# Optimization experiments

Measured on AMD Instinct MI355X. Metric: run time of the kernel, lower is better.

## Reference

```python
import jax, jax.numpy as jnp
import numpy as np

N, F_IN, H, C = 100000, 256, 128, 64
E, EP = 1600000, 500000


def setup_inputs() -> dict:
    key = jax.random.key(0)
    ks = jax.random.split(key, 8)
    x = jax.random.normal(ks[0], (N, F_IN), jnp.float32)
    masked_nodes = jax.random.randint(ks[1], (1000,), 0, N)
    pos_edge_index = jax.random.randint(ks[2], (2, EP), 0, N)
    neg_edge_index = jax.random.randint(ks[3], (2, EP), 0, N)
    edge_index = jax.random.randint(ks[4], (2, E), 0, N)
    W1 = jax.random.normal(ks[5], (F_IN, H), jnp.float32) / np.sqrt(F_IN).astype(np.float32)
    b1 = jnp.zeros((H,), jnp.float32)
    W2 = jax.random.normal(ks[6], (H, C), jnp.float32) / np.sqrt(H).astype(np.float32)
    b2 = jnp.zeros((C,), jnp.float32)
    return dict(x=x, masked_nodes=masked_nodes, pos_edge_index=pos_edge_index,
                neg_edge_index=neg_edge_index, edge_index=edge_index,
                W1=W1, b1=b1, W2=W2, b2=b2)


def gcn_conv(x, W, b, src, dst, n):
    # PyG GCNConv: h = x @ W; symmetric norm with self-loops; aggregate; + bias
    h = x @ W  # [N, out]
    deg = jax.ops.segment_sum(jnp.ones(src.shape[0], h.dtype), dst, num_segments=n) + 1.0
    dis = jax.lax.rsqrt(deg)  # D^{-1/2} including self-loop
    msg = h[src] * (dis[src] * dis[dst])[:, None]           # gather + edge-norm
    agg = jax.ops.segment_sum(msg, dst, num_segments=n)      # scatter-add
    agg = agg + h * (dis * dis)[:, None]                      # self-loop term
    return agg + b


def reference(x, masked_nodes, pos_edge_index, neg_edge_index, edge_index, W1, b1, W2, b2):
    n = x.shape[0]
    src, dst = edge_index[0], edge_index[1]
    h = jax.nn.relu(gcn_conv(x, W1, b1, src, dst, n))
    h = gcn_conv(h, W2, b2, src, dst, n)  # [N, C]
    tei = jnp.concatenate([pos_edge_index, neg_edge_index], axis=-1)  # [2, 2*EP]
    x_j = h[tei[0]]  # [2EP, C]
    x_i = h[tei[1]]
    scores = jnp.einsum('ef,ef->e', x_i, x_j)
    return scores, jnp.zeros(tei.shape, jnp.float32)
```

## Files before the change

### kernel.cpp

```cpp
#include <hip/hip_runtime.h>

#define N_NODES 100000
#define F_IN    256
#define H_DIM   128
#define C_DIM   64
#define E_EDGES 1600000
#define EP_EDGES 500000

#define NBUK 391
#define EPB  4096

typedef unsigned short bf16_t;
typedef short  short8  __attribute__((ext_vector_type(8)));
typedef float  float4v __attribute__((ext_vector_type(4)));
typedef _Float16 half8v __attribute__((ext_vector_type(8)));

__device__ inline bf16_t f2bf(float f) {
    unsigned u = __float_as_uint(f);
    u += 0x7fff + ((u >> 16) & 1);
    return (bf16_t)(u >> 16);
}
__device__ inline float bf2f(bf16_t h) {
    return __uint_as_float(((unsigned)h) << 16);
}
__device__ inline void split8(const float* vv, short* h, short* l) {
#pragma unroll
    for (int j = 0; j < 8; ++j) {
        bf16_t hb = f2bf(vv[j]);
        h[j] = (short)hb;
        l[j] = (short)f2bf(vv[j] - bf2f(hb));
    }
}
__device__ inline float4v mfma16(short8 a, short8 b, float4v c) {
    return __builtin_amdgcn_mfma_f32_16x16x32_bf16(a, b, c, 0, 0, 0);
}

__global__ __launch_bounds__(256) void bhist_kernel(const int* __restrict__ dst,
                                                    int* __restrict__ bsize) {
    __shared__ int hist[NBUK];
    const int t = threadIdx.x;
    for (int b = t; b < NBUK; b += 256) hist[b] = 0;
    __syncthreads();
    const int e0 = blockIdx.x * EPB;
#pragma unroll
    for (int i = 0; i < 16; ++i) {
        int e = e0 + i * 256 + t;
        if (e < E_EDGES) atomicAdd(&hist[dst[e] >> 8], 1);
    }
    __syncthreads();
    for (int b = t; b < NBUK; b += 256)
        if (hist[b]) atomicAdd(&bsize[b], hist[b]);
}

__global__ __launch_bounds__(512) void bscan_kernel(const int* __restrict__ bsize,
                                                    int* __restrict__ bbase,
                                                    int* __restrict__ bcursor) {
    __shared__ int sh[512];
    int t = threadIdx.x;
    sh[t] = (t < NBUK) ? bsize[t] : 0;
    __syncthreads();
#pragma unroll
    for (int off = 1; off < 512; off <<= 1) {
        int u = (t >= off) ? sh[t - off] : 0;
        __syncthreads();
        sh[t] += u;
        __syncthreads();
    }
    if (t < NBUK) {
        int ex = (t == 0) ? 0 : sh[t - 1];
        bbase[t] = ex;
        bcursor[t] = ex;
    }
    if (t == 0) bbase[NBUK] = E_EDGES;
}

__global__ __launch_bounds__(256) void bucket_scatter_kernel(const int* __restrict__ src,
                                                             const int* __restrict__ dst,
                                                             int* __restrict__ bcursor,
                                                             int2* __restrict__ pairs) {
    __shared__ int hist[NBUK];
    __shared__ int base[NBUK];
    const int t = threadIdx.x;
    for (int b = t; b < NBUK; b += 256) hist[b] = 0;
    __syncthreads();

    const int e0 = blockIdx.x * EPB;
    int s[16], d[16];
#pragma unroll
    for (int i = 0; i < 16; ++i) {
        int e = e0 + i * 256 + t;
        if (e < E_EDGES) {
            s[i] = src[e];
            d[i] = dst[e];
            atomicAdd(&hist[d[i] >> 8], 1);
        } else {
            d[i] = -1;
        }
    }
    __syncthreads();
    for (int b = t; b < NBUK; b += 256) {
        int c = hist[b];
        base[b] = c ? atomicAdd(&bcursor[b], c) : 0;
        hist[b] = 0;
    }
    __syncthreads();
#pragma unroll
    for (int i = 0; i < 16; ++i) {
        if (d[i] >= 0) {
            int b = d[i] >> 8;
            int r = atomicAdd(&hist[b], 1);
            pairs[base[b] + r] = make_int2(s[i], d[i]);
        }
    }
}

__global__ __launch_bounds__(256) void bucket_sort_kernel(const int2* __restrict__ pairs,
                                                          const int* __restrict__ bbase,
                                                          int* __restrict__ row_ptr,
                                                          float* __restrict__ dis,
                                                          int* __restrict__ csr_src) {
    __shared__ int cnt[256];
    __shared__ int sh[256];
    __shared__ int cur[256];
    const int b = blockIdx.x;
    const int node0 = b << 8;
    const int t = threadIdx.x;
    const int nn = min(256, N_NODES - node0);
    const int beg = bbase[b], end = bbase[b + 1];
    cnt[t] = 0;
    __syncthreads();
    for (int e = beg + t; e < end; e += 256)
        atomicAdd(&cnt[pairs[e].y - node0], 1);
    __syncthreads();
    int c = cnt[t];
    if (t < nn) dis[node0 + t] = rsqrtf((float)c + 1.0f);
    sh[t] = c;
    __syncthreads();
#pragma unroll
    for (int off = 1; off < 256; off <<= 1) {
        int u = (t >= off) ? sh[t - off] : 0;
        __syncthreads();
        sh[t] += u;
        __syncthreads();
    }
    int start = beg + sh[t] - c;
    if (t < nn) row_ptr[node0 + t] = start;
    cur[t] = start;
    if (b == NBUK - 1 && t == 0) row_ptr[N_NODES] = E_EDGES;
    __syncthreads();
    for (int e = beg + t; e < end; e += 256) {
        int2 p = pairs[e];
        int j = atomicAdd(&cur[p.y - node0], 1);
        csr_src[j] = p.x;
    }
}

__global__ __launch_bounds__(256) void wprep_kernel(const float* __restrict__ W1,
                                                    const float* __restrict__ W2,
                                                    short* __restrict__ w1h,
                                                    short* __restrict__ w1l,
                                                    short* __restrict__ w2h,
                                                    short* __restrict__ w2l) {
    int idx = blockIdx.x * 256 + threadIdx.x;
    if (idx < H_DIM * F_IN) {
        int n = idx >> 8, k = idx & 255;
        float w = W1[k * H_DIM + n];
        bf16_t h = f2bf(w);
        w1h[idx] = (short)h;
        w1l[idx] = (short)f2bf(w - bf2f(h));
    }
    int i2 = idx - H_DIM * F_IN;
    if (i2 >= 0 && i2 < C_DIM * H_DIM) {
        int n = i2 >> 7, k = i2 & 127;
        float w = W2[k * C_DIM + n];
        bf16_t h = f2bf(w);
        w2h[i2] = (short)h;
        w2l[i2] = (short)f2bf(w - bf2f(h));
    }
}

#define LSTR 40
__global__ __launch_bounds__(256, 3) void gemm1_mfma(const float* __restrict__ X,
                                                     const short* __restrict__ Wth,
                                                     const short* __restrict__ Wtl,
                                                     const float* __restrict__ dis,
                                                     bf16_t* __restrict__ T,
                                                     int nrows) {
    __shared__ short Bh[128 * LSTR], Bl[128 * LSTR];
    const int t = threadIdx.x;
    const int row0 = blockIdx.x * 128;
    const int w = t >> 6;
    const int lane = t & 63;
    const int m = lane & 15;
    const int q = lane >> 4;
    const int koff = q * 8;

    const int r0 = row0 + w * 32 + m;
    const int r1 = r0 + 16;
    const bool ok0 = r0 < nrows;
    const bool ok1 = r1 < nrows;
    const float* X0 = X + (long long)r0 * F_IN + q * 8;
    const float* X1 = X + (long long)r1 * F_IN + q * 8;

    float4v acc[2][8];
#pragma unroll
    for (int i = 0; i < 2; ++i)
#pragma unroll
        for (int j = 0; j < 8; ++j) acc[i][j] = {0.f, 0.f, 0.f, 0.f};

#pragma unroll 2
    for (int ks = 0; ks < 8; ++ks) {
        const int k0 = ks * 32;
#pragma unroll
        for (int i = 0; i < 2; ++i) {
            int c = t + i * 256;
            int n = c >> 2, kc = c & 3;
            *(short8*)&Bh[n * LSTR + kc * 8] = *(const short8*)&Wth[n * F_IN + k0 + kc * 8];
            *(short8*)&Bl[n * LSTR + kc * 8] = *(const short8*)&Wtl[n * F_IN + k0 + kc * 8];
        }
        float a0[8] = {0.f, 0.f, 0.f, 0.f, 0.f, 0.f, 0.f, 0.f};
        float a1[8] = {0.f, 0.f, 0.f, 0.f, 0.f, 0.f, 0.f, 0.f};
        if (ok0) {
            *(float4*)&a0[0] = *(const float4*)&X0[k0];
            *(float4*)&a0[4] = *(const float4*)&X0[k0 + 4];
        }
        if (ok1) {
            *(float4*)&a1[0] = *(const float4*)&X1[k0];
            *(float4*)&a1[4] = *(const float4*)&X1[k0 + 4];
        }
        short8 ah0, al0, ah1, al1;
        split8(a0, (short*)&ah0, (short*)&al0);
        split8(a1, (short*)&ah1, (short*)&al1);
        __syncthreads();
#pragma unroll
        for (int nc = 0; nc < 8; ++nc) {
            short8 bh = *(const short8*)&Bh[(nc * 16 + m) * LSTR + koff];
            short8 bl = *(const short8*)&Bl[(nc * 16 + m) * LSTR + koff];
            acc[0][nc] = mfma16(ah0, bh, acc[0][nc]);
            acc[0][nc] = mfma16(al0, bh, acc[0][nc]);
            acc[0][nc] = mfma16(ah0, bl, acc[0][nc]);
            acc[1][nc] = mfma16(ah1, bh, acc[1][nc]);
            acc[1][nc] = mfma16(al1, bh, acc[1][nc]);
            acc[1][nc] = mfma16(ah1, bl, acc[1][nc]);
        }
        __syncthreads();
    }
    float ds[2][4];
#pragma unroll
    for (int mt = 0; mt < 2; ++mt)
#pragma unroll
        for (int reg = 0; reg < 4; ++reg) {
            int grow = row0 + w * 32 + mt * 16 + q * 4 + reg;
            ds[mt][reg] = (grow < nrows) ? dis[grow] : 0.f;
        }
#pragma unroll
    for (int mt = 0; mt < 2; ++mt)
#pragma unroll
        for (int nc = 0; nc < 8; ++nc)
#pragma unroll
            for (int reg = 0; reg < 4; ++reg) {
                int grow = row0 + w * 32 + mt * 16 + q * 4 + reg;
                int gcol = nc * 16 + m;
                if (grow < nrows)
                    T[(long long)grow * H_DIM + gcol] = f2bf(acc[mt][nc][reg] * ds[mt][reg]);
            }
}

__global__ __launch_bounds__(256) void gemm2_mfma(const float* __restrict__ A,
                                                  const float* __restrict__ b1,
                                                  const short* __restrict__ Wth,
                                                  const short* __restrict__ Wtl,
                                                  const float* __restrict__ dis,
                                                  bf16_t* __restrict__ T,
                                                  int nrows) {
    __shared__ short Bh[64 * LSTR], Bl[64 * LSTR];
    const int t = threadIdx.x;
    const int row0 = blockIdx.x * 128;
    const int w = t >> 6;
    const int lane = t & 63;
    const int m = lane & 15;
    const int q = lane >> 4;
    const int koff = q * 8;

    const int r0 = row0 + w * 32 + m;
    const int r1 = r0 + 16;
    const bool ok0 = r0 < nrows;
    const bool ok1 = r1 < nrows;
    const float* A0 = A + (long long)r0 * H_DIM + q * 8;
    const float* A1 = A + (long long)r1 * H_DIM + q * 8;
    const float* bp = b1 + q * 8;

    float4v acc[2][4];
#pragma unroll
    for (int i = 0; i < 2; ++i)
#pragma unroll
        for (int j = 0; j < 4; ++j) acc[i][j] = {0.f, 0.f, 0.f, 0.f};

#pragma unroll 2
    for (int ks = 0; ks < 4; ++ks) {
        const int k0 = ks * 32;
        {
            int n = t >> 2, kc = t & 3;
            *(short8*)&Bh[n * LSTR + kc * 8] = *(const short8*)&Wth[n * H_DIM + k0 + kc * 8];
            *(short8*)&Bl[n * LSTR + kc * 8] = *(const short8*)&Wtl[n * H_DIM + k0 + kc * 8];
        }
        float4 bv0 = *(const float4*)&bp[k0];
        float4 bv1 = *(const float4*)&bp[k0 + 4];
        float a0[8] = {0.f, 0.f, 0.f, 0.f, 0.f, 0.f, 0.f, 0.f};
        float a1[8] = {0.f, 0.f, 0.f, 0.f, 0.f, 0.f, 0.f, 0.f};
        if (ok0) {
            float4 v0 = *(const float4*)&A0[k0];
            float4 v1 = *(const float4*)&A0[k0 + 4];
            a0[0] = fmaxf(v0.x + bv0.x, 0.f); a0[1] = fmaxf(v0.y + bv0.y, 0.f);
            a0[2] = fmaxf(v0.z + bv0.z, 0.f); a0[3] = fmaxf(v0.w + bv0.w, 0.f);
            a0[4] = fmaxf(v1.x + bv1.x, 0.f); a0[5] = fmaxf(v1.y + bv1.y, 0.f);
            a0[6] = fmaxf(v1.z + bv1.z, 0.f); a0[7] = fmaxf(v1.w + bv1.w, 0.f);
        }
        if (ok1) {
            float4 v0 = *(const float4*)&A1[k0];
            float4 v1 = *(const float4*)&A1[k0 + 4];
            a1[0] = fmaxf(v0.x + bv0.x, 0.f); a1[1] = fmaxf(v0.y + bv0.y, 0.f);
            a1[2] = fmaxf(v0.z + bv0.z, 0.f); a1[3] = fmaxf(v0.w + bv0.w, 0.f);
            a1[4] = fmaxf(v1.x + bv1.x, 0.f); a1[5] = fmaxf(v1.y + bv1.y, 0.f);
            a1[6] = fmaxf(v1.z + bv1.z, 0.f); a1[7] = fmaxf(v1.w + bv1.w, 0.f);
        }
        short8 ah0, al0, ah1, al1;
        split8(a0, (short*)&ah0, (short*)&al0);
        split8(a1, (short*)&ah1, (short*)&al1);
        __syncthreads();
#pragma unroll
        for (int nc = 0; nc < 4; ++nc) {
            short8 bh = *(const short8*)&Bh[(nc * 16 + m) * LSTR + koff];
            short8 bl = *(const short8*)&Bl[(nc * 16 + m) * LSTR + koff];
            acc[0][nc] = mfma16(ah0, bh, acc[0][nc]);
            acc[0][nc] = mfma16(al0, bh, acc[0][nc]);
            acc[0][nc] = mfma16(ah0, bl, acc[0][nc]);
            acc[1][nc] = mfma16(ah1, bh, acc[1][nc]);
            acc[1][nc] = mfma16(al1, bh, acc[1][nc]);
            acc[1][nc] = mfma16(ah1, bl, acc[1][nc]);
        }
        __syncthreads();
    }
    float ds[2][4];
#pragma unroll
    for (int mt = 0; mt < 2; ++mt)
#pragma unroll
        for (int reg = 0; reg < 4; ++reg) {
            int grow = row0 + w * 32 + mt * 16 + q * 4 + reg;
            ds[mt][reg] = (grow < nrows) ? dis[grow] : 0.f;
        }
#pragma unroll
    for (int mt = 0; mt < 2; ++mt)
#pragma unroll
        for (int nc = 0; nc < 4; ++nc)
#pragma unroll
            for (int reg = 0; reg < 4; ++reg) {
                int grow = row0 + w * 32 + mt * 16 + q * 4 + reg;
                int gcol = nc * 16 + m;
                if (grow < nrows)
                    T[(long long)grow * C_DIM + gcol] = f2bf(acc[mt][nc][reg] * ds[mt][reg]);
            }
}

__device__ inline void add8_bf16(float* acc, uint4 u) {
#pragma unroll
    for (int p = 0; p < 4; ++p) {
        unsigned w = (&u.x)[p];
        acc[2 * p]     += __uint_as_float(w << 16);
        acc[2 * p + 1] += __uint_as_float(w & 0xffff0000u);
    }
}

template <int CS, bool HAS_BIAS, bool F16OUT>
__global__ __launch_bounds__(256) void agg_kernel(const bf16_t* __restrict__ t,
                                                  const float* __restrict__ dis,
                                                  const int* __restrict__ row_ptr,
                                                  const int* __restrict__ csr_src,
                                                  const float* __restrict__ bias,
                                                  float* __restrict__ aggf,
                                                  _Float16* __restrict__ aggh) {
    unsigned idx = blockIdx.x * 256u + threadIdx.x;
    if (idx >= (unsigned)(N_NODES << CS)) return;
    int node = idx >> CS;
    int q = idx & ((1 << CS) - 1);
    const uint4* tv = (const uint4*)t;
    int beg = row_ptr[node], end = row_ptr[node + 1];

    float acc[8];
    {
        uint4 u = tv[idx];
#pragma unroll
        for (int p = 0; p < 4; ++p) {
            unsigned w = (&u.x)[p];
            acc[2 * p]     = __uint_as_float(w << 16);
            acc[2 * p + 1] = __uint_as_float(w & 0xffff0000u);
        }
    }

    int j = beg;
    for (; j + 3 < end; j += 4) {
        int s0 = csr_src[j + 0], s1 = csr_src[j + 1];
        int s2 = csr_src[j + 2], s3 = csr_src[j + 3];
        uint4 u0 = tv[((unsigned)s0 << CS) + q];
        uint4 u1 = tv[((unsigned)s1 << CS) + q];
        uint4 u2 = tv[((unsigned)s2 << CS) + q];
        uint4 u3 = tv[((unsigned)s3 << CS) + q];
        add8_bf16(acc, u0);
        add8_bf16(acc, u1);
        add8_bf16(acc, u2);
        add8_bf16(acc, u3);
    }
    for (; j < end; ++j) {
        int s = csr_src[j];
        add8_bf16(acc, tv[((unsigned)s << CS) + q]);
    }

    float dd = dis[node];
#pragma unroll
    for (int p = 0; p < 8; ++p) acc[p] *= dd;

    if (HAS_BIAS) {
        float4 bv0 = ((const float4*)bias)[q * 2];
        float4 bv1 = ((const float4*)bias)[q * 2 + 1];
        acc[0] += bv0.x; acc[1] += bv0.y; acc[2] += bv0.z; acc[3] += bv0.w;
        acc[4] += bv1.x; acc[5] += bv1.y; acc[6] += bv1.z; acc[7] += bv1.w;
    }
    if (F16OUT) {
        half8v hv;
#pragma unroll
        for (int p = 0; p < 8; ++p) hv[p] = (_Float16)acc[p];
        ((half8v*)aggh)[idx] = hv;
    } else {
        float4 o0 = make_float4(acc[0], acc[1], acc[2], acc[3]);
        float4 o1 = make_float4(acc[4], acc[5], acc[6], acc[7]);
        ((float4*)aggf)[idx * 2]     = o0;
        ((float4*)aggf)[idx * 2 + 1] = o1;
    }
}

__global__ __launch_bounds__(256) void score_kernel(const _Float16* __restrict__ h2,
                                                    const int* __restrict__ pos,
                                                    const int* __restrict__ neg,
                                                    float* __restrict__ out) {
    int tid = blockIdx.x * 256 + threadIdx.x;
    int e = tid >> 3;
    int q = tid & 7;
    if (e >= 2 * EP_EDGES) return;
    int i, j;
    if (e < EP_EDGES) {
        j = pos[e];
        i = pos[EP_EDGES + e];
    } else {
        j = neg[e - EP_EDGES];
        i = neg[e];
    }
    half8v a = ((const half8v*)h2)[i * 8 + q];
    half8v b = ((const half8v*)h2)[j * 8 + q];
    float v = 0.f;
#pragma unroll
    for (int k = 0; k < 8; ++k) v = fmaf((float)a[k], (float)b[k], v);
    v += __shfl_down(v, 4, 8);
    v += __shfl_down(v, 2, 8);
    v += __shfl_down(v, 1, 8);
    if (q == 0) out[e] = v;
}

extern "C" void kernel_launch(void* const* d_in, const int* in_sizes, int n_in,
                              void* d_out, int out_size, void* d_ws, size_t ws_size,
                              hipStream_t stream) {
    const float* x  = (const float*)d_in[0];
    const int* pos  = (const int*)d_in[2];
    const int* neg  = (const int*)d_in[3];
    const int* ei   = (const int*)d_in[4];
    const float* W1 = (const float*)d_in[5];
    const float* b1 = (const float*)d_in[6];
    const float* W2 = (const float*)d_in[7];
    const float* b2 = (const float*)d_in[8];
    float* out = (float*)d_out;

    char* ws = (char*)d_ws;
    float*  dis     = (float*) (ws + 0);
    int*    row_ptr = (int*)   (ws + 400000);
    int*    bsize   = (int*)   (ws + 800128);
    int*    bbase   = (int*)   (ws + 801792);
    int*    bcursor = (int*)   (ws + 803456);
    int*    csr_src = (int*)   (ws + 805120);
    int2*   pairs   = (int2*)  (ws + 7205120);
    _Float16* h2f16 = (_Float16*)(ws + 7205120);
    bf16_t* t       = (bf16_t*)(ws + 20005120);
    float*  agg     = (float*) (ws + 45605120);
    short*  w1th    = (short*) (ws + 96805120);
    short*  w1tl    = (short*) (ws + 96870656);
    short*  w2th    = (short*) (ws + 96936192);
    short*  w2tl    = (short*) (ws + 96952576);

    const int* esrc = ei;
    const int* edst = ei + E_EDGES;

    hipMemsetAsync(bsize, 0, NBUK * sizeof(int), stream);
    bhist_kernel<<<(E_EDGES + EPB - 1) / EPB, 256, 0, stream>>>(edst, bsize);
    bscan_kernel<<<1, 512, 0, stream>>>(bsize, bbase, bcursor);
    bucket_scatter_kernel<<<(E_EDGES + EPB - 1) / EPB, 256, 0, stream>>>(
        esrc, edst, bcursor, pairs);
    bucket_sort_kernel<<<NBUK, 256, 0, stream>>>(pairs, bbase, row_ptr, dis, csr_src);
    wprep_kernel<<<(H_DIM * F_IN + C_DIM * H_DIM + 255) / 256, 256, 0, stream>>>(
        W1, W2, w1th, w1tl, w2th, w2tl);

    gemm1_mfma<<<(N_NODES + 127) / 128, 256, 0, stream>>>(x, w1th, w1tl, dis, t, N_NODES);
    agg_kernel<4, false, false><<<(N_NODES * 16 + 255) / 256, 256, 0, stream>>>(
        t, dis, row_ptr, csr_src, nullptr, agg, nullptr);

    gemm2_mfma<<<(N_NODES + 127) / 128, 256, 0, stream>>>(agg, b1, w2th, w2tl, dis, t, N_NODES);
    agg_kernel<3, true, true><<<(N_NODES * 8 + 255) / 256, 256, 0, stream>>>(
        t, dis, row_ptr, csr_src, b2, nullptr, h2f16);

    score_kernel<<<(2 * EP_EDGES * 8) / 256, 256, 0, stream>>>(h2f16, pos, neg, out);

    hipMemsetAsync(out + 2 * EP_EDGES, 0, (size_t)4 * EP_EDGES * sizeof(float), stream);
}
```

Baseline: 403.3 us.

## Double-buffer GEMM weight tiles via direct global-to-LDS loads with swizzled layout

Both MFMA GEMM kernels now double-buffer the weight tiles in LDS and prefetch the next K-slice of weights and activations while the current slice is computed, dropping one barrier per iteration. Weight staging uses the global_load_lds builtin so data goes straight into shared memory without passing through registers. To avoid LDS bank conflicts without padding, the weight prep kernel writes an XOR-swizzled column order that the readers undo. This costs more LDS and registers per block and gives gemm2 a 3-block occupancy hint, and the overall gain is limited because the GEMMs are only part of a pipeline that also includes graph aggregation.

```diff
diff --git a/kernel.cpp b/kernel.cpp
--- a/kernel.cpp
+++ b/kernel.cpp
@@ -34,6 +34,12 @@
 __device__ inline float4v mfma16(short8 a, short8 b, float4v c) {
     return __builtin_amdgcn_mfma_f32_16x16x32_bf16(a, b, c, 0, 0, 0);
 }
+__device__ inline void gload_lds16(const void* gptr, void* lptr) {
+    __builtin_amdgcn_global_load_lds(
+        (const __attribute__((address_space(1))) unsigned int*)gptr,
+        (__attribute__((address_space(3))) unsigned int*)lptr, 16, 0, 0);
+}
+#define XSWZ(nn) (((nn) >> 1) & 3)
 
 __global__ __launch_bounds__(256) void bhist_kernel(const int* __restrict__ dst,
                                                     int* __restrict__ bsize) {
@@ -164,36 +170,58 @@
     int idx = blockIdx.x * 256 + threadIdx.x;
     if (idx < H_DIM * F_IN) {
         int n = idx >> 8, k = idx & 255;
+        int kc = (k >> 3) & 3;
+        int dk = (k & ~0x18) | (((kc ^ XSWZ(n)) & 3) << 3);
         float w = W1[k * H_DIM + n];
         bf16_t h = f2bf(w);
-        w1h[idx] = (short)h;
-        w1l[idx] = (short)f2bf(w - bf2f(h));
+        w1h[n * F_IN + dk] = (short)h;
+        w1l[n * F_IN + dk] = (short)f2bf(w - bf2f(h));
     }
     int i2 = idx - H_DIM * F_IN;
     if (i2 >= 0 && i2 < C_DIM * H_DIM) {
         int n = i2 >> 7, k = i2 & 127;
+        int kc = (k >> 3) & 3;
+        int dk = (k & ~0x18) | (((kc ^ XSWZ(n)) & 3) << 3);
         float w = W2[k * C_DIM + n];
         bf16_t h = f2bf(w);
-        w2h[i2] = (short)h;
-        w2l[i2] = (short)f2bf(w - bf2f(h));
-    }
-}
-
-#define LSTR 40
+        w2h[n * H_DIM + dk] = (short)h;
+        w2l[n * H_DIM + dk] = (short)f2bf(w - bf2f(h));
+    }
+}
+
+#define G1_STAGE(BUF, KSN)                                                     \
+    for (int i_ = 0; i_ < 2; ++i_) {                                           \
+        int e_ = t + i_ * 256;                                                 \
+        gload_lds16(&Wth[(e_ >> 2) * F_IN + (KSN) * 32 + (e_ & 3) * 8],        \
+                    &Bh[(BUF) * 4096 + e_ * 8]);                               \
+        gload_lds16(&Wtl[(e_ >> 2) * F_IN + (KSN) * 32 + (e_ & 3) * 8],        \
+                    &Bl[(BUF) * 4096 + e_ * 8]);                               \
+    }
+
+#define G1_LOADA(BANK, KSN)                                                    \
+    if (ok0) {                                                                 \
+        *(float4*)&aP[BANK][0][0] = *(const float4*)&X0[(KSN) * 32];           \
+        *(float4*)&aP[BANK][0][4] = *(const float4*)&X0[(KSN) * 32 + 4];       \
+    }                                                                          \
+    if (ok1) {                                                                 \
+        *(float4*)&aP[BANK][1][0] = *(const float4*)&X1[(KSN) * 32];           \
+        *(float4*)&aP[BANK][1][4] = *(const float4*)&X1[(KSN) * 32 + 4];       \
+    }
+
 __global__ __launch_bounds__(256, 3) void gemm1_mfma(const float* __restrict__ X,
                                                      const short* __restrict__ Wth,
                                                      const short* __restrict__ Wtl,
                                                      const float* __restrict__ dis,
                                                      bf16_t* __restrict__ T,
                                                      int nrows) {
-    __shared__ short Bh[128 * LSTR], Bl[128 * LSTR];
+    __shared__ short Bh[2 * 4096], Bl[2 * 4096];
     const int t = threadIdx.x;
     const int row0 = blockIdx.x * 128;
     const int w = t >> 6;
     const int lane = t & 63;
     const int m = lane & 15;
     const int q = lane >> 4;
-    const int koff = q * 8;
+    const int qs = ((q ^ XSWZ(m)) & 3) << 3;
 
     const int r0 = row0 + w * 32 + m;
     const int r1 = r0 + 16;
@@ -208,34 +236,27 @@
 #pragma unroll
         for (int j = 0; j < 8; ++j) acc[i][j] = {0.f, 0.f, 0.f, 0.f};
 
-#pragma unroll 2
+    float aP[2][2][8] = {};
+
+    G1_STAGE(0, 0)
+    G1_LOADA(0, 0)
+    __syncthreads();
+
+#pragma unroll
     for (int ks = 0; ks < 8; ++ks) {
-        const int k0 = ks * 32;
-#pragma unroll
-        for (int i = 0; i < 2; ++i) {
-            int c = t + i * 256;
-            int n = c >> 2, kc = c & 3;
-            *(short8*)&Bh[n * LSTR + kc * 8] = *(const short8*)&Wth[n * F_IN + k0 + kc * 8];
-            *(short8*)&Bl[n * LSTR + kc * 8] = *(const short8*)&Wtl[n * F_IN + k0 + kc * 8];
-        }
-        float a0[8] = {0.f, 0.f, 0.f, 0.f, 0.f, 0.f, 0.f, 0.f};
-        float a1[8] = {0.f, 0.f, 0.f, 0.f, 0.f, 0.f, 0.f, 0.f};
-        if (ok0) {
-            *(float4*)&a0[0] = *(const float4*)&X0[k0];
-            *(float4*)&a0[4] = *(const float4*)&X0[k0 + 4];
-        }
-        if (ok1) {
-            *(float4*)&a1[0] = *(const float4*)&X1[k0];
-            *(float4*)&a1[4] = *(const float4*)&X1[k0 + 4];
+        const int p = ks & 1;
+        if (ks < 7) {
+            G1_STAGE(p ^ 1, ks + 1)
+            G1_LOADA(p ^ 1, ks + 1)
         }
         short8 ah0, al0, ah1, al1;
-        split8(a0, (short*)&ah0, (short*)&al0);
-        split8(a1, (short*)&ah1, (short*)&al1);
-        __syncthreads();
+        split8(aP[p][0], (short*)&ah0, (short*)&al0);
+        split8(aP[p][1], (short*)&ah1, (short*)&al1);
 #pragma unroll
         for (int nc = 0; nc < 8; ++nc) {
-            short8 bh = *(const short8*)&Bh[(nc * 16 + m) * LSTR + koff];
-            short8 bl = *(const short8*)&Bl[(nc * 16 + m) * LSTR + koff];
+            const int bo = p * 4096 + (nc * 16 + m) * 32 + qs;
+            short8 bh = *(const short8*)&Bh[bo];
+            short8 bl = *(const short8*)&Bl[bo];
             acc[0][nc] = mfma16(ah0, bh, acc[0][nc]);
             acc[0][nc] = mfma16(al0, bh, acc[0][nc]);
             acc[0][nc] = mfma16(ah0, bl, acc[0][nc]);
@@ -245,13 +266,13 @@
         }
         __syncthreads();
     }
-    float ds[2][4];
+    float ds_[2][4];
 #pragma unroll
     for (int mt = 0; mt < 2; ++mt)
 #pragma unroll
         for (int reg = 0; reg < 4; ++reg) {
             int grow = row0 + w * 32 + mt * 16 + q * 4 + reg;
-            ds[mt][reg] = (grow < nrows) ? dis[grow] : 0.f;
+            ds_[mt][reg] = (grow < nrows) ? dis[grow] : 0.f;
         }
 #pragma unroll
     for (int mt = 0; mt < 2; ++mt)
@@ -262,25 +283,41 @@
                 int grow = row0 + w * 32 + mt * 16 + q * 4 + reg;
                 int gcol = nc * 16 + m;
                 if (grow < nrows)
-                    T[(long long)grow * H_DIM + gcol] = f2bf(acc[mt][nc][reg] * ds[mt][reg]);
+                    T[(long long)grow * H_DIM + gcol] = f2bf(acc[mt][nc][reg] * ds_[mt][reg]);
             }
 }
 
-__global__ __launch_bounds__(256) void gemm2_mfma(const float* __restrict__ A,
-                                                  const float* __restrict__ b1,
-                                                  const short* __restrict__ Wth,
-                                                  const short* __restrict__ Wtl,
-                                                  const float* __restrict__ dis,
-                                                  bf16_t* __restrict__ T,
-                                                  int nrows) {
-    __shared__ short Bh[64 * LSTR], Bl[64 * LSTR];
+#define G2_STAGE(BUF, KSN)                                                     \
+    gload_lds16(&Wth[(t >> 2) * H_DIM + (KSN) * 32 + (t & 3) * 8],             \
+                &Bh[(BUF) * 2048 + t * 8]);                                    \
+    gload_lds16(&Wtl[(t >> 2) * H_DIM + (KSN) * 32 + (t & 3) * 8],             \
+                &Bl[(BUF) * 2048 + t * 8]);
+
+#define G2_LOADA(BANK, KSN)                                                    \
+    if (ok0) {                                                                 \
+        *(float4*)&aP[BANK][0][0] = *(const float4*)&A0[(KSN) * 32];           \
+        *(float4*)&aP[BANK][0][4] = *(const float4*)&A0[(KSN) * 32 + 4];       \
+    }                                                                          \
+    if (ok1) {                                                                 \
+        *(float4*)&aP[BANK][1][0] = *(const float4*)&A1[(KSN) * 32];           \
+        *(float4*)&aP[BANK][1][4] = *(const float4*)&A1[(KSN) * 32 + 4];       \
+    }
+
+__global__ __launch_bounds__(256, 3) void gemm2_mfma(const float* __restrict__ A,
+                                                     const float* __restrict__ b1,
+                                                     const short* __restrict__ Wth,
+                                                     const short* __restrict__ Wtl,
+                                                     const float* __restrict__ dis,
+                                                     bf16_t* __restrict__ T,
+                                                     int nrows) {
+    __shared__ short Bh[2 * 2048], Bl[2 * 2048];
     const int t = threadIdx.x;
     const int row0 = blockIdx.x * 128;
     const int w = t >> 6;
     const int lane = t & 63;
     const int m = lane & 15;
     const int q = lane >> 4;
-    const int koff = q * 8;
+    const int qs = ((q ^ XSWZ(m)) & 3) << 3;
 
     const int r0 = row0 + w * 32 + m;
     const int r1 = r0 + 16;
@@ -296,42 +333,38 @@
 #pragma unroll
         for (int j = 0; j < 4; ++j) acc[i][j] = {0.f, 0.f, 0.f, 0.f};
 
-#pragma unroll 2
+    float aP[2][2][8] = {};
+
+    G2_STAGE(0, 0)
+    G2_LOADA(0, 0)
+    __syncthreads();
+
+#pragma unroll
     for (int ks = 0; ks < 4; ++ks) {
-        const int k0 = ks * 32;
-        {
-            int n = t >> 2, kc = t & 3;
-            *(short8*)&Bh[n * LSTR + kc * 8] = *(const short8*)&Wth[n * H_DIM + k0 + kc * 8];
-            *(short8*)&Bl[n * LSTR + kc * 8] = *(const short8*)&Wtl[n * H_DIM + k0 + kc * 8];
-        }
-        float4 bv0 = *(const float4*)&bp[k0];
-        float4 bv1 = *(const float4*)&bp[k0 + 4];
-        float a0[8] = {0.f, 0.f, 0.f, 0.f, 0.f, 0.f, 0.f, 0.f};
-        float a1[8] = {0.f, 0.f, 0.f, 0.f, 0.f, 0.f, 0.f, 0.f};
-        if (ok0) {
-            float4 v0 = *(const float4*)&A0[k0];
-            float4 v1 = *(const float4*)&A0[k0 + 4];
-            a0[0] = fmaxf(v0.x + bv0.x, 0.f); a0[1] = fmaxf(v0.y + bv0.y, 0.f);
-            a0[2] = fmaxf(v0.z + bv0.z, 0.f); a0[3] = fmaxf(v0.w + bv0.w, 0.f);
-            a0[4] = fmaxf(v1.x + bv1.x, 0.f); a0[5] = fmaxf(v1.y + bv1.y, 0.f);
-            a0[6] = fmaxf(v1.z + bv1.z, 0.f); a0[7] = fmaxf(v1.w + bv1.w, 0.f);
-        }
-        if (ok1) {
-            float4 v0 = *(const float4*)&A1[k0];
-            float4 v1 = *(const float4*)&A1[k0 + 4];
-            a1[0] = fmaxf(v0.x + bv0.x, 0.f); a1[1] = fmaxf(v0.y + bv0.y, 0.f);
-            a1[2] = fmaxf(v0.z + bv0.z, 0.f); a1[3] = fmaxf(v0.w + bv0.w, 0.f);
-            a1[4] = fmaxf(v1.x + bv1.x, 0.f); a1[5] = fmaxf(v1.y + bv1.y, 0.f);
-            a1[6] = fmaxf(v1.z + bv1.z, 0.f); a1[7] = fmaxf(v1.w + bv1.w, 0.f);
-        }
+        const int p = ks & 1;
+        if (ks < 3) {
+            G2_STAGE(p ^ 1, ks + 1)
+            G2_LOADA(p ^ 1, ks + 1)
+        }
+        float4 bv0 = *(const float4*)&bp[ks * 32];
+        float4 bv1 = *(const float4*)&bp[ks * 32 + 4];
+        float a0[8], a1[8];
+        a0[0] = fmaxf(aP[p][0][0] + bv0.x, 0.f); a0[1] = fmaxf(aP[p][0][1] + bv0.y, 0.f);
+        a0[2] = fmaxf(aP[p][0][2] + bv0.z, 0.f); a0[3] = fmaxf(aP[p][0][3] + bv0.w, 0.f);
+        a0[4] = fmaxf(aP[p][0][4] + bv1.x, 0.f); a0[5] = fmaxf(aP[p][0][5] + bv1.y, 0.f);
+        a0[6] = fmaxf(aP[p][0][6] + bv1.z, 0.f); a0[7] = fmaxf(aP[p][0][7] + bv1.w, 0.f);
+        a1[0] = fmaxf(aP[p][1][0] + bv0.x, 0.f); a1[1] = fmaxf(aP[p][1][1] + bv0.y, 0.f);
+        a1[2] = fmaxf(aP[p][1][2] + bv0.z, 0.f); a1[3] = fmaxf(aP[p][1][3] + bv0.w, 0.f);
+        a1[4] = fmaxf(aP[p][1][4] + bv1.x, 0.f); a1[5] = fmaxf(aP[p][1][5] + bv1.y, 0.f);
+        a1[6] = fmaxf(aP[p][1][6] + bv1.z, 0.f); a1[7] = fmaxf(aP[p][1][7] + bv1.w, 0.f);
         short8 ah0, al0, ah1, al1;
         split8(a0, (short*)&ah0, (short*)&al0);
         split8(a1, (short*)&ah1, (short*)&al1);
-        __syncthreads();
 #pragma unroll
         for (int nc = 0; nc < 4; ++nc) {
-            short8 bh = *(const short8*)&Bh[(nc * 16 + m) * LSTR + koff];
-            short8 bl = *(const short8*)&Bl[(nc * 16 + m) * LSTR + koff];
+            const int bo = p * 2048 + (nc * 16 + m) * 32 + qs;
+            short8 bh = *(const short8*)&Bh[bo];
+            short8 bl = *(const short8*)&Bl[bo];
             acc[0][nc] = mfma16(ah0, bh, acc[0][nc]);
             acc[0][nc] = mfma16(al0, bh, acc[0][nc]);
             acc[0][nc] = mfma16(ah0, bl, acc[0][nc]);
@@ -341,13 +374,13 @@
         }
         __syncthreads();
     }
-    float ds[2][4];
+    float ds_[2][4];
 #pragma unroll
     for (int mt = 0; mt < 2; ++mt)
 #pragma unroll
         for (int reg = 0; reg < 4; ++reg) {
             int grow = row0 + w * 32 + mt * 16 + q * 4 + reg;
-            ds[mt][reg] = (grow < nrows) ? dis[grow] : 0.f;
+            ds_[mt][reg] = (grow < nrows) ? dis[grow] : 0.f;
         }
 #pragma unroll
     for (int mt = 0; mt < 2; ++mt)
@@ -358,7 +391,7 @@
                 int grow = row0 + w * 32 + mt * 16 + q * 4 + reg;
                 int gcol = nc * 16 + m;
                 if (grow < nrows)
-                    T[(long long)grow * C_DIM + gcol] = f2bf(acc[mt][nc][reg] * ds[mt][reg]);
+                    T[(long long)grow * C_DIM + gcol] = f2bf(acc[mt][nc][reg] * ds_[mt][reg]);
             }
 }
 
```

New measurement: 400.3 us. No clear change (-0.8%).
